# Kernel tuning notes

Hardware: AMD Instinct MI355X
Metric: run time of the kernel (lower is better)

The kernel has to match this reference:

```python
import jax, jax.numpy as jnp
import numpy as np

N_NODE, N_USER = 100000, 30000
N_REL, N_BASIS = 8, 30
EMB, OUT = 32, 32
E = 1600000
BATCH = 16384
H1, H2, H3 = 64, 32, 16
NEG_SLOPE = 0.2


def setup_inputs() -> dict:
    key = jax.random.key(0)
    ks = jax.random.split(key, 20)
    g = lambda k, shape: jax.random.normal(k, shape, dtype=jnp.float32) * 0.05
    inp = {
        "x_ids": jnp.arange(N_NODE, dtype=jnp.int64 if jax.config.jax_enable_x64 else jnp.int32),
        "edge_index": jax.random.randint(ks[0], (2, E), 0, N_NODE),
        "edge_type": jax.random.randint(ks[1], (E,), 0, N_REL),
        "users": jax.random.randint(ks[2], (BATCH,), 0, N_USER),
        "bundles": jax.random.randint(ks[3], (BATCH,), 0, N_NODE),
        # parameters
        "emb": g(ks[4], (N_NODE, EMB)),
        "basis": g(ks[5], (N_BASIS, EMB, OUT)),
        "weight": g(ks[6], (N_REL, N_BASIS)),
        "att": g(ks[7], (N_REL, 2 * OUT)),
        "root": g(ks[8], (EMB, OUT)),
        "bias": jnp.zeros((OUT,), jnp.float32),
        "W1": g(ks[9], (2 * OUT, H1)), "b1": jnp.zeros((H1,), jnp.float32),
        "W2": g(ks[10], (H1, H2)), "b2": jnp.zeros((H2,), jnp.float32),
        "W3": g(ks[11], (H2, H3)), "b3": jnp.zeros((H3,), jnp.float32),
        "Wo": g(ks[12], (H3, 1)), "bo": jnp.zeros((1,), jnp.float32),
    }
    return inp


def _tgcn_fwd(x_ids, edge_index, edge_type, users, bundles,
              emb, basis, weight, att, root, bias,
              W1, b1, W2, b2, W3, b3, Wo, bo):
    N = emb.shape[0]
    R = weight.shape[0]
    O = basis.shape[2]
    x = emb[x_ids]                                   # (N, F) embedding lookup
    # basis decomposition: (R, F, O)
    w = (weight @ basis.reshape(N_BASIS, -1)).reshape(R, EMB, O)
    # transform every node under every relation once, then gather per edge
    xh = jnp.einsum('nf,rfo->nro', x, w)             # (N, R, O)
    src, dst = edge_index[0], edge_index[1]          # j (source), i (target)
    h_i = xh[dst, edge_type]                         # (E, O)
    h_j = xh[src, edge_type]                         # (E, O)
    a = att[edge_type]                               # (E, 2O)
    alpha = (h_i * a[:, :O]).sum(-1) + (h_j * a[:, O:]).sum(-1)
    alpha = jax.nn.leaky_relu(alpha, NEG_SLOPE)
    # segment softmax keyed by (target node, relation)
    seg_key = dst * R + edge_type
    n_seg = N * R
    amax = jax.ops.segment_max(alpha, seg_key, num_segments=n_seg)
    ex = jnp.exp(alpha - amax[seg_key])
    denom = jax.ops.segment_sum(ex, seg_key, num_segments=n_seg)
    alpha = ex / (denom[seg_key] + 1e-16)
    # scatter-add weighted messages into target nodes
    agg = jax.ops.segment_sum(h_j * alpha[:, None], dst, num_segments=N)
    h = jax.nn.relu(agg + x @ root + bias)           # update + ReLU
    z = jnp.concatenate([h[users], h[bundles]], axis=1)  # (B, 2O)
    z = jax.nn.relu(z @ W1 + b1)
    z = jax.nn.relu(z @ W2 + b2)
    z = jax.nn.relu(z @ W3 + b3)
    return z @ Wo + bo                               # (B, 1) logits


def reference(x_ids, edge_index, edge_type, users, bundles,
              emb, basis, weight, att, root, bias,
              W1, b1, W2, b2, W3, b3, Wo, bo):
    return _tgcn_fwd(x_ids, edge_index, edge_type, users, bundles,
                     emb, basis, weight, att, root, bias,
                     W1, b1, W2, b2, W3, b3, Wo, bo)
```

## Files before the change

### kernel.cpp

```cpp
#include <hip/hip_runtime.h>
#include <hip/hip_bf16.h>

#define N_NODE 100000
#define N_REL  8
#define EMB    32
#define OUT    32
#define N_BASIS 30
#define E_EDGE 1600000
#define BATCH  16384
#define H1 64
#define H2 32
#define H3 16
#define NEG_SLOPE 0.2f

#define BSH   8
#define NBKT  391
#define BCAP  5120
#define PCH   2048

#define K5T   128

#define NPB   32
#define K1GRID (N_NODE / NPB)
#define RTS   36


__global__ __launch_bounds__(256) void k0f(const float* __restrict__ weight,
                                           const float* __restrict__ basis,
                                           const float* __restrict__ att,
                                           float* __restrict__ w,
                                           float* __restrict__ wa,
                                           unsigned* __restrict__ bcnt) {
    __shared__ float wl[N_REL * EMB * OUT];
    int t = threadIdx.x;
    for (int i = t; i < N_REL * EMB * OUT; i += 256) {
        int r = i >> 10, fo = i & 1023;
        float acc = 0.f;
        #pragma unroll
        for (int b = 0; b < N_BASIS; b++)
            acc = fmaf(weight[r * N_BASIS + b], basis[b * (EMB * OUT) + fo], acc);
        wl[i] = acc;
        w[i] = acc;
    }
    __syncthreads();
    for (int i = t; i < 512; i += 256) {
        int which = i >> 8, rf = i & 255, r = rf >> 5, f = rf & 31;
        const float* wrow = wl + (r * 32 + f) * 32;
        const float* arow = att + r * 64 + which * 32;
        float acc = 0.f;
        #pragma unroll
        for (int o = 0; o < 32; o++) acc = fmaf(wrow[o], arow[o], acc);
        wa[i] = acc;
    }
    for (int i = t; i < NBKT; i += 256) bcnt[i] = 0;
}

__global__ __launch_bounds__(256) void k1x(const float* __restrict__ emb,
                                           const float* __restrict__ w,
                                           const float* __restrict__ wa,
                                           const float* __restrict__ root,
                                           const float* __restrict__ bias,
                                           unsigned short* __restrict__ xh,
                                           float* __restrict__ p_i,
                                           float* __restrict__ p_j,
                                           float* __restrict__ agg) {
    __shared__ float xs[NPB * EMB];
    __shared__ float rootsT[OUT * RTS];
    __shared__ float was[16 * RTS];
    __shared__ float biass[OUT];

    const int t = threadIdx.x;
    const int n0 = blockIdx.x * NPB;

    const int ro = t & 127;
    const int rhi = ro >> 5, olo = ro & 31;
    float wc0[EMB], wc1[EMB];
    #pragma unroll
    for (int f = 0; f < EMB; f++) {
        wc0[f] = w[rhi * 1024 + f * 32 + olo];
        wc1[f] = w[rhi * 1024 + 4096 + f * 32 + olo];
    }
    #pragma unroll
    for (int f = 0; f < EMB; f++) asm volatile("" : "+v"(wc0[f]), "+v"(wc1[f]));

    ((float4*)xs)[t] = ((const float4*)(emb + (size_t)n0 * EMB))[t];
    for (int i = t; i < EMB * OUT; i += 256) {
        int f = i >> 5, oo = i & 31;
        rootsT[oo * RTS + f] = root[i];
    }
    for (int i = t; i < 512; i += 256) {
        int which = i >> 8, r = (i >> 5) & 7, f = i & 31;
        was[(which * 8 + r) * RTS + f] = wa[i];
    }
    if (t < OUT) biass[t] = bias[t];
    __syncthreads();

    {
        const int n = t >> 3, r = t & 7;
        const float4* xr = (const float4*)&xs[n * EMB];
        const float4* wi = (const float4*)&was[r * RTS];
        const float4* wj = (const float4*)&was[(8 + r) * RTS];
        float ai = 0.f, aj = 0.f;
        #pragma unroll
        for (int c = 0; c < 8; c++) {
            float4 xv = xr[c];
            float4 vi = wi[c], vj = wj[c];
            ai = fmaf(xv.x, vi.x, ai); ai = fmaf(xv.y, vi.y, ai);
            ai = fmaf(xv.z, vi.z, ai); ai = fmaf(xv.w, vi.w, ai);
            aj = fmaf(xv.x, vj.x, aj); aj = fmaf(xv.y, vj.y, aj);
            aj = fmaf(xv.z, vj.z, aj); aj = fmaf(xv.w, vj.w, aj);
        }
        p_i[n0 * N_REL + t] = ai;
        p_j[n0 * N_REL + t] = aj;
    }

    {
        const int o = t & 31, ng = t >> 5;
        const float4* rt = (const float4*)&rootsT[o * RTS];
        float4 r0 = rt[0], r1 = rt[1], r2 = rt[2], r3 = rt[3];
        float4 r4 = rt[4], r5 = rt[5], r6 = rt[6], r7 = rt[7];
        float bv = biass[o];
        #pragma unroll
        for (int q = 0; q < 4; q++) {
            int n = ng * 4 + q;
            const float4* xr = (const float4*)&xs[n * EMB];
            float g = bv;
            float4 xv;
            xv = xr[0]; g = fmaf(xv.x, r0.x, g); g = fmaf(xv.y, r0.y, g);
                        g = fmaf(xv.z, r0.z, g); g = fmaf(xv.w, r0.w, g);
            xv = xr[1]; g = fmaf(xv.x, r1.x, g); g = fmaf(xv.y, r1.y, g);
                        g = fmaf(xv.z, r1.z, g); g = fmaf(xv.w, r1.w, g);
            xv = xr[2]; g = fmaf(xv.x, r2.x, g); g = fmaf(xv.y, r2.y, g);
                        g = fmaf(xv.z, r2.z, g); g = fmaf(xv.w, r2.w, g);
            xv = xr[3]; g = fmaf(xv.x, r3.x, g); g = fmaf(xv.y, r3.y, g);
                        g = fmaf(xv.z, r3.z, g); g = fmaf(xv.w, r3.w, g);
            xv = xr[4]; g = fmaf(xv.x, r4.x, g); g = fmaf(xv.y, r4.y, g);
                        g = fmaf(xv.z, r4.z, g); g = fmaf(xv.w, r4.w, g);
            xv = xr[5]; g = fmaf(xv.x, r5.x, g); g = fmaf(xv.y, r5.y, g);
                        g = fmaf(xv.z, r5.z, g); g = fmaf(xv.w, r5.w, g);
            xv = xr[6]; g = fmaf(xv.x, r6.x, g); g = fmaf(xv.y, r6.y, g);
                        g = fmaf(xv.z, r6.z, g); g = fmaf(xv.w, r6.w, g);
            xv = xr[7]; g = fmaf(xv.x, r7.x, g); g = fmaf(xv.y, r7.y, g);
                        g = fmaf(xv.z, r7.z, g); g = fmaf(xv.w, r7.w, g);
            agg[(size_t)(n0 + n) * OUT + o] = g;
        }
    }

    {
        const int half = t >> 7;
        #pragma unroll 4
        for (int s = 0; s < 16; s++) {
            int n = 2 * s + half;
            const float4* xr = (const float4*)&xs[n * EMB];
            float a0 = 0.f, a1 = 0.f;
            #pragma unroll
            for (int c = 0; c < 8; c++) {
                float4 xv = xr[c];
                a0 = fmaf(xv.x, wc0[4 * c + 0], a0);
                a0 = fmaf(xv.y, wc0[4 * c + 1], a0);
                a0 = fmaf(xv.z, wc0[4 * c + 2], a0);
                a0 = fmaf(xv.w, wc0[4 * c + 3], a0);
                a1 = fmaf(xv.x, wc1[4 * c + 0], a1);
                a1 = fmaf(xv.y, wc1[4 * c + 1], a1);
                a1 = fmaf(xv.z, wc1[4 * c + 2], a1);
                a1 = fmaf(xv.w, wc1[4 * c + 3], a1);
            }
            __hip_bfloat16 b0 = __float2bfloat16(a0);
            __hip_bfloat16 b1 = __float2bfloat16(a1);
            unsigned short* xp = xh + (size_t)(n0 + n) * 256;
            xp[ro]       = *(unsigned short*)&b0;
            xp[ro + 128] = *(unsigned short*)&b1;
        }
    }
}

__global__ __launch_bounds__(256) void k_part(const int* __restrict__ src,
                                              const int* __restrict__ dst,
                                              const int* __restrict__ et,
                                              unsigned* __restrict__ bcnt,
                                              unsigned* __restrict__ part) {
    __shared__ unsigned long long stage[PCH];
    __shared__ unsigned hist[NBKT], lbase[NBKT], lcur[NBKT], gbase[NBKT];
    __shared__ unsigned sc[256];
    int t = threadIdx.x;
    for (int i = t; i < NBKT; i += 256) hist[i] = 0;
    __syncthreads();
    int beg = blockIdx.x * PCH, end = min(beg + PCH, E_EDGE);
    int n = end - beg;
    int ng = n >> 2;
    int g0 = t, g1 = t + 256;
    bool has0 = g0 < ng, has1 = g1 < ng;
    int4 s0v = {}, d0v = {}, e0v = {}, s1v = {}, d1v = {}, e1v = {};
    if (has0) {
        s0v = *(const int4*)&src[beg + 4 * g0];
        d0v = *(const int4*)&dst[beg + 4 * g0];
        e0v = *(const int4*)&et[beg + 4 * g0];
    }
    if (has1) {
        s1v = *(const int4*)&src[beg + 4 * g1];
        d1v = *(const int4*)&dst[beg + 4 * g1];
        e1v = *(const int4*)&et[beg + 4 * g1];
    }
    if (has0) {
        atomicAdd(&hist[(unsigned)d0v.x >> BSH], 1u);
        atomicAdd(&hist[(unsigned)d0v.y >> BSH], 1u);
        atomicAdd(&hist[(unsigned)d0v.z >> BSH], 1u);
        atomicAdd(&hist[(unsigned)d0v.w >> BSH], 1u);
    }
    if (has1) {
        atomicAdd(&hist[(unsigned)d1v.x >> BSH], 1u);
        atomicAdd(&hist[(unsigned)d1v.y >> BSH], 1u);
        atomicAdd(&hist[(unsigned)d1v.z >> BSH], 1u);
        atomicAdd(&hist[(unsigned)d1v.w >> BSH], 1u);
    }
    __syncthreads();
    unsigned v0 = (2 * t < NBKT) ? hist[2 * t] : 0u;
    unsigned v1 = (2 * t + 1 < NBKT) ? hist[2 * t + 1] : 0u;
    unsigned s = v0 + v1;
    sc[t] = s;
    __syncthreads();
    for (int off = 1; off < 256; off <<= 1) {
        unsigned y = (t >= off) ? sc[t - off] : 0u;
        __syncthreads();
        sc[t] += y;
        __syncthreads();
    }
    unsigned ex = sc[t] - s;
    if (2 * t < NBKT)     { lbase[2 * t] = ex;          lcur[2 * t] = ex; }
    if (2 * t + 1 < NBKT) { lbase[2 * t + 1] = ex + v0; lcur[2 * t + 1] = ex + v0; }
    __syncthreads();
    #define K_PART_STAGE(dd, ss, ee) do {                                   \
        unsigned b_ = (unsigned)(dd) >> BSH;                                \
        unsigned ent_ = ((unsigned)((dd) & 255) << 20)                      \
                      | ((unsigned)(ss) << 3) | (unsigned)(ee);             \
        unsigned pos_ = atomicAdd(&lcur[b_], 1u);                           \
        stage[pos_] = ((unsigned long long)b_ << 32) | ent_; } while (0)
    if (has0) {
        K_PART_STAGE(d0v.x, s0v.x, e0v.x);
        K_PART_STAGE(d0v.y, s0v.y, e0v.y);
        K_PART_STAGE(d0v.z, s0v.z, e0v.z);
        K_PART_STAGE(d0v.w, s0v.w, e0v.w);
    }
    if (has1) {
        K_PART_STAGE(d1v.x, s1v.x, e1v.x);
        K_PART_STAGE(d1v.y, s1v.y, e1v.y);
        K_PART_STAGE(d1v.z, s1v.z, e1v.z);
        K_PART_STAGE(d1v.w, s1v.w, e1v.w);
    }
    #undef K_PART_STAGE
    __syncthreads();
    for (int i = t; i < NBKT; i += 256)
        if (hist[i]) gbase[i] = atomicAdd(&bcnt[i], hist[i]);
    __syncthreads();
    for (int i = t; i < n; i += 256) {
        unsigned long long s64 = stage[i];
        unsigned b = (unsigned)(s64 >> 32);
        unsigned ent = (unsigned)s64;
        part[b * BCAP + gbase[b] + (i - lbase[b])] = ent;
    }
}

__global__ __launch_bounds__(256) void k_sort(const unsigned* __restrict__ bcnt,
                                              const unsigned* __restrict__ part,
                                              int* __restrict__ payload,
                                              int* __restrict__ begp,
                                              int* __restrict__ endp) {
    __shared__ unsigned ent[BCAP];
    __shared__ unsigned ent2[BCAP];
    __shared__ unsigned hist[256], dbase[256], dcur[256];
    __shared__ unsigned sc[256];
    int t = threadIdx.x;
    int b = blockIdx.x;
    unsigned s0 = (unsigned)b * BCAP;
    int n = (int)bcnt[b];
    if (n > BCAP) n = BCAP;
    hist[t] = 0;
    __syncthreads();
    int n4 = n & ~3;
    for (int i = 4 * t; i < n4; i += 1024) {
        uint4 e4 = *(const uint4*)&part[s0 + i];
        ent[i + 0] = e4.x; atomicAdd(&hist[e4.x >> 20], 1u);
        ent[i + 1] = e4.y; atomicAdd(&hist[e4.y >> 20], 1u);
        ent[i + 2] = e4.z; atomicAdd(&hist[e4.z >> 20], 1u);
        ent[i + 3] = e4.w; atomicAdd(&hist[e4.w >> 20], 1u);
    }
    for (int i = n4 + t; i < n; i += 256) {
        unsigned e = part[s0 + i];
        ent[i] = e;
        atomicAdd(&hist[e >> 20], 1u);
    }
    __syncthreads();
    unsigned v = hist[t];
    sc[t] = v;
    __syncthreads();
    for (int off = 1; off < 256; off <<= 1) {
        unsigned y = (t >= off) ? sc[t - off] : 0u;
        __syncthreads();
        sc[t] += y;
        __syncthreads();
    }
    unsigned ex = sc[t] - v;
    dbase[t] = ex;
    dcur[t] = ex;
    __syncthreads();
    int d = (b << BSH) + t;
    if (d < N_NODE) {
        begp[d] = (int)(s0 + dbase[t]);
        endp[d] = (int)(s0 + dbase[t] + hist[t]);
    }
    for (int i = t; i < n; i += 256) {
        unsigned e = ent[i];
        unsigned pos = atomicAdd(&dcur[e >> 20], 1u);
        ent2[pos] = e & 0xFFFFFu;
    }
    __syncthreads();
    for (int i = 4 * t; i < n4; i += 1024) {
        uint4 o4 = { ent2[i + 0], ent2[i + 1], ent2[i + 2], ent2[i + 3] };
        *(uint4*)&payload[s0 + i] = o4;
    }
    for (int i = n4 + t; i < n; i += 256) payload[s0 + i] = (int)ent2[i];
}

__global__ __launch_bounds__(256) void k_agg(const int* __restrict__ begp,
                                             const int* __restrict__ endp,
                                             const int* __restrict__ payload,
                                             const float* __restrict__ p_i,
                                             const float* __restrict__ p_j,
                                             const unsigned short* __restrict__ xh,
                                             float* __restrict__ agg,
                                             int d0, int d1) {
    int d = d0 + blockIdx.x * 4 + (threadIdx.x >> 6);
    if (d >= d1) return;
    const int lane = threadIdx.x & 63;
    const int h = lane >> 5;
    const int o = lane & 31;
    const int beg = begp[d], end = endp[d];
    const int cnt = end - beg;
    if (cnt == 0) return;

    float pid[8];
    #pragma unroll
    for (int k = 0; k < 8; k++) pid[k] = p_i[(d << 3) | k];

    if (cnt <= 64) {
        int sr = 0, r = 0; float ev = 0.f;
        if (lane < cnt) {
            sr = payload[beg + lane];
            r = sr & 7;
            float pi = pid[0];
            #pragma unroll
            for (int k = 1; k < 8; k++) pi = (r == k) ? pid[k] : pi;
            float a = pi + p_j[sr];
            a = (a >= 0.f) ? a : NEG_SLOPE * a;
            ev = __expf(a);
        }
        float sex[8];
        #pragma unroll
        for (int k = 0; k < 8; k++) sex[k] = (r == k) ? ev : 0.f;
        #pragma unroll
        for (int k = 0; k < 8; k++) {
            #pragma unroll
            for (int m = 1; m <= 32; m <<= 1) sex[k] += __shfl_xor(sex[k], m, 64);
        }
        float de = sex[0];
        #pragma unroll
        for (int k = 1; k < 8; k++) de = (r == k) ? sex[k] : de;
        float al = ev / (de + 1e-16f);

        float w0 = 0.f, w1 = 0.f, w2 = 0.f, w3 = 0.f;
        for (int j0 = 0; j0 < cnt; j0 += 8) {
            float b0 = __shfl(al, j0 + h,     64);
            float b1 = __shfl(al, j0 + 2 + h, 64);
            float b2 = __shfl(al, j0 + 4 + h, 64);
            float b3 = __shfl(al, j0 + 6 + h, 64);
            int t0 = payload[beg + j0 + h]     & 0xFFFFF;
            int t1 = payload[beg + j0 + 2 + h] & 0xFFFFF;
            int t2 = payload[beg + j0 + 4 + h] & 0xFFFFF;
            int t3 = payload[beg + j0 + 6 + h] & 0xFFFFF;
            float x0 = __uint_as_float((unsigned)xh[((unsigned)t0 << 5) + o] << 16);
            float x1 = __uint_as_float((unsigned)xh[((unsigned)t1 << 5) + o] << 16);
            float x2 = __uint_as_float((unsigned)xh[((unsigned)t2 << 5) + o] << 16);
            float x3 = __uint_as_float((unsigned)xh[((unsigned)t3 << 5) + o] << 16);
            w0 = fmaf(b0, x0, w0); w1 = fmaf(b1, x1, w1);
            w2 = fmaf(b2, x2, w2); w3 = fmaf(b3, x3, w3);
        }
        float vv = (w0 + w1) + (w2 + w3);
        vv += __shfl_xor(vv, 32, 64);
        if (h == 0) agg[(size_t)d * OUT + o] += vv;
        return;
    }

    float sex[8] = {0.f,0.f,0.f,0.f,0.f,0.f,0.f,0.f};
    for (int i = beg + lane; i < end; i += 64) {
        int sr = payload[i];
        int r = sr & 7;
        float pi = pid[0];
        #pragma unroll
        for (int k = 1; k < 8; k++) pi = (r == k) ? pid[k] : pi;
        float a = pi + p_j[sr];
        a = (a >= 0.f) ? a : NEG_SLOPE * a;
        float ev = __expf(a);
        #pragma unroll
        for (int k = 0; k < 8; k++) sex[k] += (r == k) ? ev : 0.f;
    }
    #pragma unroll
    for (int k = 0; k < 8; k++) {
        #pragma unroll
        for (int m = 1; m <= 32; m <<= 1) sex[k] += __shfl_xor(sex[k], m, 64);
    }
    float v0 = 0.f;
    for (int c = beg; c < end; c += 64) {
        int i = c + lane;
        int sr = 0; float al = 0.f;
        if (i < end) {
            sr = payload[i];
            int r = sr & 7;
            float pi = pid[0];
            #pragma unroll
            for (int k = 1; k < 8; k++) pi = (r == k) ? pid[k] : pi;
            float a = pi + p_j[sr];
            a = (a >= 0.f) ? a : NEG_SLOPE * a;
            float ev = __expf(a);
            float de = sex[0];
            #pragma unroll
            for (int k = 1; k < 8; k++) de = (r == k) ? sex[k] : de;
            al = ev / (de + 1e-16f);
        }
        int m = min(64, end - c);
        for (int j0 = 0; j0 < m; j0 += 2) {
            int e0 = j0 + h;
            float a0 = __shfl(al, e0, 64); int s0 = __shfl(sr, e0, 64);
            if (e0 < m) {
                float xv = __uint_as_float((unsigned)xh[((unsigned)s0 << 5) + o] << 16);
                v0 = fmaf(a0, xv, v0);
            }
        }
    }
    float vv = v0;
    vv += __shfl_xor(vv, 32, 64);
    if (h == 0) agg[(size_t)d * OUT + o] += vv;
}

__global__ __launch_bounds__(K5T, 1) void k5_mlp(const int* __restrict__ users,
                                                 const int* __restrict__ bundles,
                                                 const float* __restrict__ agg,
                                                 const float* __restrict__ W1,
                                                 const float* __restrict__ b1,
                                                 const float* __restrict__ W2,
                                                 const float* __restrict__ b2,
                                                 const float* __restrict__ W3,
                                                 const float* __restrict__ b3,
                                                 const float* __restrict__ Wo,
                                                 const float* __restrict__ bo,
                                                 float* __restrict__ out) {
    __shared__ float4 W1s[2 * OUT * H1 / 4];
    __shared__ float4 W2s[H1 * H2 / 4];
    __shared__ float4 W3s[H2 * H3 / 4];
    __shared__ float b1s[H1], b2s[H2], b3s[H3], Wos[H3];
    __shared__ float bos;
    __shared__ float zs[K5T * 65];
    __shared__ float h1s[K5T * 65];
    const int t = threadIdx.x;

    const float4* W14 = (const float4*)W1;
    const float4* W24 = (const float4*)W2;
    const float4* W34 = (const float4*)W3;
    for (int i = t; i < 1024; i += K5T) W1s[i] = W14[i];
    for (int i = t; i < 512; i += K5T) W2s[i] = W24[i];
    for (int i = t; i < 128; i += K5T) W3s[i] = W34[i];
    if (t < H1) b1s[t] = b1[t];
    if (t < H2) b2s[t] = b2[t];
    if (t < H3) { b3s[t] = b3[t]; Wos[t] = Wo[t]; }
    if (t == 0) bos = bo[0];

    const int item = blockIdx.x * K5T + t;
    const int u = users[item], v = bundles[item];
    const float4* av = (const float4*)agg;
    float* zrow = &zs[t * 65];
    float* h1row = &h1s[t * 65];

    #pragma unroll
    for (int c = 0; c < 8; c++) {
        float4 x = av[(size_t)u * 8 + c];
        zrow[4 * c + 0] = fmaxf(x.x, 0.f); zrow[4 * c + 1] = fmaxf(x.y, 0.f);
        zrow[4 * c + 2] = fmaxf(x.z, 0.f); zrow[4 * c + 3] = fmaxf(x.w, 0.f);
    }
    #pragma unroll
    for (int c = 0; c < 8; c++) {
        float4 x = av[(size_t)v * 8 + c];
        zrow[32 + 4 * c + 0] = fmaxf(x.x, 0.f); zrow[32 + 4 * c + 1] = fmaxf(x.y, 0.f);
        zrow[32 + 4 * c + 2] = fmaxf(x.z, 0.f); zrow[32 + 4 * c + 3] = fmaxf(x.w, 0.f);
    }
    __syncthreads();

    #pragma unroll 4
    for (int j4 = 0; j4 < 16; j4++) {
        float a0 = b1s[4 * j4 + 0], a1 = b1s[4 * j4 + 1];
        float a2 = b1s[4 * j4 + 2], a3 = b1s[4 * j4 + 3];
        #pragma unroll 16
        for (int k = 0; k < 2 * OUT; k++) {
            float zk = zrow[k];
            float4 wv = W1s[k * 16 + j4];
            a0 = fmaf(zk, wv.x, a0); a1 = fmaf(zk, wv.y, a1);
            a2 = fmaf(zk, wv.z, a2); a3 = fmaf(zk, wv.w, a3);
        }
        h1row[4 * j4 + 0] = fmaxf(a0, 0.f); h1row[4 * j4 + 1] = fmaxf(a1, 0.f);
        h1row[4 * j4 + 2] = fmaxf(a2, 0.f); h1row[4 * j4 + 3] = fmaxf(a3, 0.f);
    }

    #pragma unroll 4
    for (int j4 = 0; j4 < 8; j4++) {
        float a0 = b2s[4 * j4 + 0], a1 = b2s[4 * j4 + 1];
        float a2 = b2s[4 * j4 + 2], a3 = b2s[4 * j4 + 3];
        #pragma unroll 16
        for (int k = 0; k < H1; k++) {
            float hk = h1row[k];
            float4 wv = W2s[k * 8 + j4];
            a0 = fmaf(hk, wv.x, a0); a1 = fmaf(hk, wv.y, a1);
            a2 = fmaf(hk, wv.z, a2); a3 = fmaf(hk, wv.w, a3);
        }
        zrow[4 * j4 + 0] = fmaxf(a0, 0.f); zrow[4 * j4 + 1] = fmaxf(a1, 0.f);
        zrow[4 * j4 + 2] = fmaxf(a2, 0.f); zrow[4 * j4 + 3] = fmaxf(a3, 0.f);
    }

    float h3v[16];
    #pragma unroll
    for (int j4 = 0; j4 < 4; j4++) {
        float a0 = b3s[4 * j4 + 0], a1 = b3s[4 * j4 + 1];
        float a2 = b3s[4 * j4 + 2], a3 = b3s[4 * j4 + 3];
        #pragma unroll 16
        for (int k = 0; k < H2; k++) {
            float hk = zrow[k];
            float4 wv = W3s[k * 4 + j4];
            a0 = fmaf(hk, wv.x, a0); a1 = fmaf(hk, wv.y, a1);
            a2 = fmaf(hk, wv.z, a2); a3 = fmaf(hk, wv.w, a3);
        }
        h3v[4 * j4 + 0] = fmaxf(a0, 0.f); h3v[4 * j4 + 1] = fmaxf(a1, 0.f);
        h3v[4 * j4 + 2] = fmaxf(a2, 0.f); h3v[4 * j4 + 3] = fmaxf(a3, 0.f);
    }

    float acc = bos;
    #pragma unroll
    for (int k = 0; k < H3; k++) acc = fmaf(h3v[k], Wos[k], acc);
    out[item] = acc;
}

extern "C" void kernel_launch(void* const* d_in, const int* in_sizes, int n_in,
                              void* d_out, int out_size, void* d_ws, size_t ws_size,
                              hipStream_t stream) {
    (void)in_sizes; (void)n_in; (void)out_size; (void)ws_size;
    const int*   eidx   = (const int*)d_in[1];
    const int*   etype  = (const int*)d_in[2];
    const int*   users  = (const int*)d_in[3];
    const int*   bund   = (const int*)d_in[4];
    const float* emb    = (const float*)d_in[5];
    const float* basis  = (const float*)d_in[6];
    const float* weight = (const float*)d_in[7];
    const float* att    = (const float*)d_in[8];
    const float* root   = (const float*)d_in[9];
    const float* bias   = (const float*)d_in[10];
    const float* W1 = (const float*)d_in[11]; const float* b1 = (const float*)d_in[12];
    const float* W2 = (const float*)d_in[13]; const float* b2 = (const float*)d_in[14];
    const float* W3 = (const float*)d_in[15]; const float* b3 = (const float*)d_in[16];
    const float* Wo = (const float*)d_in[17]; const float* bo = (const float*)d_in[18];
    float* out = (float*)d_out;

    const int* src = eidx;
    const int* dst = eidx + E_EDGE;

    float* ws       = (float*)d_ws;
    float* w        = ws;
    float* wa       = w + N_REL * EMB * OUT;
    unsigned short* xh = (unsigned short*)(wa + 512);
    float* p_i      = (float*)(xh + (size_t)N_NODE * 256);
    float* p_j      = p_i + N_NODE * N_REL;
    float* agg      = p_j + N_NODE * N_REL;
    int*   payload  = (int*)(agg + (long)N_NODE * OUT);
    int*   begp     = payload + NBKT * BCAP;
    int*   endp     = begp + N_NODE;
    unsigned* bcnt  = (unsigned*)(endp + N_NODE);
    unsigned* part  = (unsigned*)agg;

    k0f<<<1, 256, 0, stream>>>(weight, basis, att, w, wa, bcnt);
    k_part<<<(E_EDGE + PCH - 1) / PCH, 256, 0, stream>>>(src, dst, etype, bcnt, part);
    k_sort<<<NBKT, 256, 0, stream>>>(bcnt, part, payload, begp, endp);
    k1x<<<K1GRID, 256, 0, stream>>>(emb, w, wa, root, bias, xh, p_i, p_j, agg);
    k_agg<<<12500, 256, 0, stream>>>(begp, endp, payload, p_i, p_j, xh, agg,
                                     0, 50000);
    k_agg<<<12500, 256, 0, stream>>>(begp, endp, payload, p_i, p_j, xh, agg,
                                     50000, 100000);
    k5_mlp<<<BATCH / K5T, K5T, 0, stream>>>(users, bund, agg, W1, b1, W2, b2, W3, b3,
                                            Wo, bo, out);
}
```

Measured before the change: 317.4 us.

## Make node-transform kernel persistent with double-buffered embedding prefetch

The per-node transform kernel now runs on a fixed grid of 782 blocks, and each block loops over tiles of 32 nodes instead of handling one tile per block. The per-block setup (64 relation-weight registers per thread, root, attention and bias tiles) is therefore paid once per block rather than once per tile. The next tile's embeddings are prefetched into registers while the current tile is computed, then written into a second shared buffer. The shared-memory row stride is padded to 36 to reduce bank conflicts, and launch bounds request 4 blocks per CU, which may constrain register allocation.

```diff
diff --git a/kernel.cpp b/kernel.cpp
--- a/kernel.cpp
+++ b/kernel.cpp
@@ -21,7 +21,9 @@
 #define K5T   128
 
 #define NPB   32
-#define K1GRID (N_NODE / NPB)
+#define NTILES (N_NODE / NPB)
+#define K1GRID 782
+#define XSS   36
 #define RTS   36
 
 
@@ -55,25 +57,24 @@
     for (int i = t; i < NBKT; i += 256) bcnt[i] = 0;
 }
 
-__global__ __launch_bounds__(256) void k1x(const float* __restrict__ emb,
-                                           const float* __restrict__ w,
-                                           const float* __restrict__ wa,
-                                           const float* __restrict__ root,
-                                           const float* __restrict__ bias,
-                                           unsigned short* __restrict__ xh,
-                                           float* __restrict__ p_i,
-                                           float* __restrict__ p_j,
-                                           float* __restrict__ agg) {
-    __shared__ float xs[NPB * EMB];
+__global__ __launch_bounds__(256, 4) void k1x(const float* __restrict__ emb,
+                                              const float* __restrict__ w,
+                                              const float* __restrict__ wa,
+                                              const float* __restrict__ root,
+                                              const float* __restrict__ bias,
+                                              unsigned short* __restrict__ xh,
+                                              float* __restrict__ p_i,
+                                              float* __restrict__ p_j,
+                                              float* __restrict__ agg) {
+    __shared__ float xs[2][NPB * XSS];
     __shared__ float rootsT[OUT * RTS];
     __shared__ float was[16 * RTS];
     __shared__ float biass[OUT];
 
     const int t = threadIdx.x;
-    const int n0 = blockIdx.x * NPB;
-
     const int ro = t & 127;
     const int rhi = ro >> 5, olo = ro & 31;
+
     float wc0[EMB], wc1[EMB];
     #pragma unroll
     for (int f = 0; f < EMB; f++) {
@@ -83,7 +84,6 @@
     #pragma unroll
     for (int f = 0; f < EMB; f++) asm volatile("" : "+v"(wc0[f]), "+v"(wc1[f]));
 
-    ((float4*)xs)[t] = ((const float4*)(emb + (size_t)n0 * EMB))[t];
     for (int i = t; i < EMB * OUT; i += 256) {
         int f = i >> 5, oo = i & 31;
         rootsT[oo * RTS + f] = root[i];
@@ -93,84 +93,107 @@
         was[(which * 8 + r) * RTS + f] = wa[i];
     }
     if (t < OUT) biass[t] = bias[t];
-    __syncthreads();
-
+
+    const int sn = t >> 3, sc = t & 7;
+    int tile = blockIdx.x;
     {
-        const int n = t >> 3, r = t & 7;
-        const float4* xr = (const float4*)&xs[n * EMB];
-        const float4* wi = (const float4*)&was[r * RTS];
-        const float4* wj = (const float4*)&was[(8 + r) * RTS];
-        float ai = 0.f, aj = 0.f;
-        #pragma unroll
-        for (int c = 0; c < 8; c++) {
-            float4 xv = xr[c];
-            float4 vi = wi[c], vj = wj[c];
-            ai = fmaf(xv.x, vi.x, ai); ai = fmaf(xv.y, vi.y, ai);
-            ai = fmaf(xv.z, vi.z, ai); ai = fmaf(xv.w, vi.w, ai);
-            aj = fmaf(xv.x, vj.x, aj); aj = fmaf(xv.y, vj.y, aj);
-            aj = fmaf(xv.z, vj.z, aj); aj = fmaf(xv.w, vj.w, aj);
-        }
-        p_i[n0 * N_REL + t] = ai;
-        p_j[n0 * N_REL + t] = aj;
-    }
-
-    {
-        const int o = t & 31, ng = t >> 5;
-        const float4* rt = (const float4*)&rootsT[o * RTS];
-        float4 r0 = rt[0], r1 = rt[1], r2 = rt[2], r3 = rt[3];
-        float4 r4 = rt[4], r5 = rt[5], r6 = rt[6], r7 = rt[7];
-        float bv = biass[o];
-        #pragma unroll
-        for (int q = 0; q < 4; q++) {
-            int n = ng * 4 + q;
-            const float4* xr = (const float4*)&xs[n * EMB];
-            float g = bv;
-            float4 xv;
-            xv = xr[0]; g = fmaf(xv.x, r0.x, g); g = fmaf(xv.y, r0.y, g);
-                        g = fmaf(xv.z, r0.z, g); g = fmaf(xv.w, r0.w, g);
-            xv = xr[1]; g = fmaf(xv.x, r1.x, g); g = fmaf(xv.y, r1.y, g);
-                        g = fmaf(xv.z, r1.z, g); g = fmaf(xv.w, r1.w, g);
-            xv = xr[2]; g = fmaf(xv.x, r2.x, g); g = fmaf(xv.y, r2.y, g);
-                        g = fmaf(xv.z, r2.z, g); g = fmaf(xv.w, r2.w, g);
-            xv = xr[3]; g = fmaf(xv.x, r3.x, g); g = fmaf(xv.y, r3.y, g);
-                        g = fmaf(xv.z, r3.z, g); g = fmaf(xv.w, r3.w, g);
-            xv = xr[4]; g = fmaf(xv.x, r4.x, g); g = fmaf(xv.y, r4.y, g);
-                        g = fmaf(xv.z, r4.z, g); g = fmaf(xv.w, r4.w, g);
-            xv = xr[5]; g = fmaf(xv.x, r5.x, g); g = fmaf(xv.y, r5.y, g);
-                        g = fmaf(xv.z, r5.z, g); g = fmaf(xv.w, r5.w, g);
-            xv = xr[6]; g = fmaf(xv.x, r6.x, g); g = fmaf(xv.y, r6.y, g);
-                        g = fmaf(xv.z, r6.z, g); g = fmaf(xv.w, r6.w, g);
-            xv = xr[7]; g = fmaf(xv.x, r7.x, g); g = fmaf(xv.y, r7.y, g);
-                        g = fmaf(xv.z, r7.z, g); g = fmaf(xv.w, r7.w, g);
-            agg[(size_t)(n0 + n) * OUT + o] = g;
-        }
-    }
-
-    {
-        const int half = t >> 7;
-        #pragma unroll 4
-        for (int s = 0; s < 16; s++) {
-            int n = 2 * s + half;
-            const float4* xr = (const float4*)&xs[n * EMB];
-            float a0 = 0.f, a1 = 0.f;
+        float4 v = ((const float4*)(emb + (size_t)tile * NPB * EMB))[t];
+        *(float4*)&xs[0][sn * XSS + sc * 4] = v;
+    }
+    __syncthreads();
+
+    int buf = 0;
+    for (; tile < NTILES; tile += K1GRID) {
+        const int ntile = tile + K1GRID;
+        const bool has = ntile < NTILES;
+        float4 pf;
+        if (has)
+            pf = ((const float4*)(emb + (size_t)ntile * NPB * EMB))[t];
+
+        const int n0 = tile * NPB;
+        const float* xb = xs[buf];
+
+        {
+            const float4* xr = (const float4*)&xb[(t >> 3) * XSS];
+            const float4* wi = (const float4*)&was[(t & 7) * RTS];
+            const float4* wj = (const float4*)&was[(8 + (t & 7)) * RTS];
+            float ai = 0.f, aj = 0.f;
             #pragma unroll
             for (int c = 0; c < 8; c++) {
                 float4 xv = xr[c];
-                a0 = fmaf(xv.x, wc0[4 * c + 0], a0);
-                a0 = fmaf(xv.y, wc0[4 * c + 1], a0);
-                a0 = fmaf(xv.z, wc0[4 * c + 2], a0);
-                a0 = fmaf(xv.w, wc0[4 * c + 3], a0);
-                a1 = fmaf(xv.x, wc1[4 * c + 0], a1);
-                a1 = fmaf(xv.y, wc1[4 * c + 1], a1);
-                a1 = fmaf(xv.z, wc1[4 * c + 2], a1);
-                a1 = fmaf(xv.w, wc1[4 * c + 3], a1);
+                float4 vi = wi[c], vj = wj[c];
+                ai = fmaf(xv.x, vi.x, ai); ai = fmaf(xv.y, vi.y, ai);
+                ai = fmaf(xv.z, vi.z, ai); ai = fmaf(xv.w, vi.w, ai);
+                aj = fmaf(xv.x, vj.x, aj); aj = fmaf(xv.y, vj.y, aj);
+                aj = fmaf(xv.z, vj.z, aj); aj = fmaf(xv.w, vj.w, aj);
             }
-            __hip_bfloat16 b0 = __float2bfloat16(a0);
-            __hip_bfloat16 b1 = __float2bfloat16(a1);
-            unsigned short* xp = xh + (size_t)(n0 + n) * 256;
-            xp[ro]       = *(unsigned short*)&b0;
-            xp[ro + 128] = *(unsigned short*)&b1;
-        }
+            p_i[n0 * N_REL + t] = ai;
+            p_j[n0 * N_REL + t] = aj;
+        }
+
+        {
+            const int o = t & 31, ng = t >> 5;
+            const float4* rt = (const float4*)&rootsT[o * RTS];
+            float4 r0 = rt[0], r1 = rt[1], r2 = rt[2], r3 = rt[3];
+            float4 r4 = rt[4], r5 = rt[5], r6 = rt[6], r7 = rt[7];
+            float bv = biass[o];
+            #pragma unroll
+            for (int q = 0; q < 4; q++) {
+                int n = ng * 4 + q;
+                const float4* xr = (const float4*)&xb[n * XSS];
+                float g = bv;
+                float4 xv;
+                xv = xr[0]; g = fmaf(xv.x, r0.x, g); g = fmaf(xv.y, r0.y, g);
+                            g = fmaf(xv.z, r0.z, g); g = fmaf(xv.w, r0.w, g);
+                xv = xr[1]; g = fmaf(xv.x, r1.x, g); g = fmaf(xv.y, r1.y, g);
+                            g = fmaf(xv.z, r1.z, g); g = fmaf(xv.w, r1.w, g);
+                xv = xr[2]; g = fmaf(xv.x, r2.x, g); g = fmaf(xv.y, r2.y, g);
+                            g = fmaf(xv.z, r2.z, g); g = fmaf(xv.w, r2.w, g);
+                xv = xr[3]; g = fmaf(xv.x, r3.x, g); g = fmaf(xv.y, r3.y, g);
+                            g = fmaf(xv.z, r3.z, g); g = fmaf(xv.w, r3.w, g);
+                xv = xr[4]; g = fmaf(xv.x, r4.x, g); g = fmaf(xv.y, r4.y, g);
+                            g = fmaf(xv.z, r4.z, g); g = fmaf(xv.w, r4.w, g);
+                xv = xr[5]; g = fmaf(xv.x, r5.x, g); g = fmaf(xv.y, r5.y, g);
+                            g = fmaf(xv.z, r5.z, g); g = fmaf(xv.w, r5.w, g);
+                xv = xr[6]; g = fmaf(xv.x, r6.x, g); g = fmaf(xv.y, r6.y, g);
+                            g = fmaf(xv.z, r6.z, g); g = fmaf(xv.w, r6.w, g);
+                xv = xr[7]; g = fmaf(xv.x, r7.x, g); g = fmaf(xv.y, r7.y, g);
+                            g = fmaf(xv.z, r7.z, g); g = fmaf(xv.w, r7.w, g);
+                agg[(size_t)(n0 + n) * OUT + o] = g;
+            }
+        }
+
+        {
+            const int half = t >> 7;
+            #pragma unroll 4
+            for (int s = 0; s < 16; s++) {
+                int n = 2 * s + half;
+                const float4* xr = (const float4*)&xb[n * XSS];
+                float a0 = 0.f, a1 = 0.f;
+                #pragma unroll
+                for (int c = 0; c < 8; c++) {
+                    float4 xv = xr[c];
+                    a0 = fmaf(xv.x, wc0[4 * c + 0], a0);
+                    a0 = fmaf(xv.y, wc0[4 * c + 1], a0);
+                    a0 = fmaf(xv.z, wc0[4 * c + 2], a0);
+                    a0 = fmaf(xv.w, wc0[4 * c + 3], a0);
+                    a1 = fmaf(xv.x, wc1[4 * c + 0], a1);
+                    a1 = fmaf(xv.y, wc1[4 * c + 1], a1);
+                    a1 = fmaf(xv.z, wc1[4 * c + 2], a1);
+                    a1 = fmaf(xv.w, wc1[4 * c + 3], a1);
+                }
+                __hip_bfloat16 b0 = __float2bfloat16(a0);
+                __hip_bfloat16 b1 = __float2bfloat16(a1);
+                unsigned short* xp = xh + (size_t)(n0 + n) * 256;
+                xp[ro]       = *(unsigned short*)&b0;
+                xp[ro + 128] = *(unsigned short*)&b1;
+            }
+        }
+
+        if (has)
+            *(float4*)&xs[buf ^ 1][sn * XSS + sc * 4] = pf;
+        __syncthreads();
+        buf ^= 1;
     }
 }
 
```

Measured after the change: 611.3 us. 1.93x slower.
